# Performance work log

Hardware: AMD Instinct MI355X
Metric: run time of the kernel (lower is better)

## Reference

```python
import jax, jax.numpy as jnp
import numpy as np

N = 100000      # num_nodes
E = 1600000     # num_edges
F_IN = 10       # node_feature_dim
H = 64          # hidden_channels
B = 128         # num graphs in batch
C = 3           # num_classes
EPS = 1e-5      # BatchNorm eps


def setup_inputs() -> dict:
    key = jax.random.key(0)
    ks = jax.random.split(key, 32)
    inp = {
        'x': jax.random.normal(ks[0], (N, F_IN), dtype=jnp.float32),
        'edge_index': jax.random.randint(ks[1], (2, E), 0, N, dtype=jnp.int32),
        'batch': jnp.sort(jax.random.randint(ks[2], (N,), 0, B, dtype=jnp.int32)),
    }
    dims = [(F_IN, H), (H, H), (H, H)]
    k = 3
    for i, (din, dout) in enumerate(dims, start=1):
        inp[f'W{i}'] = jax.random.normal(ks[k], (din, dout)) * (1.0 / np.sqrt(din)); k += 1
        inp[f'b{i}'] = jax.random.normal(ks[k], (dout,)) * 0.01; k += 1
        inp[f'g{i}'] = 1.0 + 0.1 * jax.random.normal(ks[k], (dout,)); k += 1
        inp[f'be{i}'] = 0.1 * jax.random.normal(ks[k], (dout,)); k += 1
        inp[f'm{i}'] = 0.1 * jax.random.normal(ks[k], (dout,)); k += 1
        inp[f'v{i}'] = 0.5 + jax.random.uniform(ks[k], (dout,)); k += 1
    inp['fw1'] = jax.random.normal(ks[k], (H, H // 2)) * (1.0 / np.sqrt(H)); k += 1
    inp['fb1'] = jax.random.normal(ks[k], (H // 2,)) * 0.01; k += 1
    inp['fw2'] = jax.random.normal(ks[k], (H // 2, C)) * (1.0 / np.sqrt(H // 2)); k += 1
    inp['fb2'] = jax.random.normal(ks[k], (C,)) * 0.01
    return inp


def reference(x, edge_index, batch,
              W1, b1, g1, be1, m1, v1,
              W2, b2, g2, be2, m2, v2,
              W3, b3, g3, be3, m3, v3,
              fw1, fb1, fw2, fb2):
    src, dst = edge_index[0], edge_index[1]
    # GCN normalization with implicit self-loops: deg includes the self-loop
    deg = jax.ops.segment_sum(jnp.ones((E,), x.dtype), dst, num_segments=N) + 1.0
    dinv = jax.lax.rsqrt(deg)
    ecoef = (dinv[src] * dinv[dst])[:, None]   # per-edge norm [E,1]
    scoef = (dinv * dinv)[:, None]             # self-loop norm [N,1]

    def gcn_conv(h, W, b):
        h = h @ W  # [N, dout]
        agg = jax.ops.segment_sum(h[src] * ecoef, dst, num_segments=N)
        return agg + h * scoef + b

    def bn(h, g, be, m, v):  # eval-mode BatchNorm1d
        return (h - m) * jax.lax.rsqrt(v + EPS) * g + be

    h = jax.nn.relu(bn(gcn_conv(x, W1, b1), g1, be1, m1, v1))
    h = jax.nn.relu(bn(gcn_conv(h, W2, b2), g2, be2, m2, v2))
    h = jax.nn.relu(bn(gcn_conv(h, W3, b3), g3, be3, m3, v3))

    # global mean pool over batch assignment
    counts = jax.ops.segment_sum(jnp.ones((N,), h.dtype), batch, num_segments=B)
    pooled = jax.ops.segment_sum(h, batch, num_segments=B) / jnp.maximum(counts, 1.0)[:, None]

    out = jax.nn.relu(pooled @ fw1 + fb1) @ fw2 + fb2  # [B, C]
    return out
```

## Files before the change

kernel.cpp:

```cpp
#include <hip/hip_runtime.h>
#include <hip/hip_bf16.h>
#include <hip/hip_fp16.h>

#define N_NODES 100000
#define E_EDGES 1600000
#define F_IN    10
#define H       64
#define B_GR    128
#define C_CLS   3
#define BN_EPS  1e-5f
#define NH      (N_NODES * H)
#define NBLK_SCAN ((N_NODES + 255) / 256)

#define TILE1   4096
#define NB1     391
#define L2CAP   6144

__global__ void deg_kernel(const int* __restrict__ dst, int* __restrict__ deg) {
    int e = blockIdx.x * blockDim.x + threadIdx.x;
    if (e < E_EDGES) atomicAdd(&deg[dst[e]], 1);
}

__global__ void dinv_kernel(const int* __restrict__ deg, float* __restrict__ dinv) {
    int n = blockIdx.x * blockDim.x + threadIdx.x;
    if (n < N_NODES) dinv[n] = rsqrtf((float)deg[n] + 1.0f);
}

__global__ void scan1_kernel(const int* __restrict__ deg, int* __restrict__ rowptr,
                             int* __restrict__ blockSums) {
    __shared__ int lds[256];
    int t = threadIdx.x;
    int i = blockIdx.x * 256 + t;
    int v = (i < N_NODES) ? deg[i] : 0;
    lds[t] = v;
    __syncthreads();
    for (int off = 1; off < 256; off <<= 1) {
        int add = (t >= off) ? lds[t - off] : 0;
        __syncthreads();
        lds[t] += add;
        __syncthreads();
    }
    if (i < N_NODES) rowptr[i] = lds[t] - v;
    if (t == 255) blockSums[blockIdx.x] = lds[255];
}

__global__ void scan2_kernel(const int* __restrict__ blockSums, int* __restrict__ blockOff) {
    __shared__ int lds[512];
    int t = threadIdx.x;
    int v = (t < NBLK_SCAN) ? blockSums[t] : 0;
    lds[t] = v;
    __syncthreads();
    for (int off = 1; off < 512; off <<= 1) {
        int add = (t >= off) ? lds[t - off] : 0;
        __syncthreads();
        lds[t] += add;
        __syncthreads();
    }
    if (t < NBLK_SCAN) blockOff[t] = lds[t] - v;
}

__global__ void scan3_kernel(int* __restrict__ rowptr, const int* __restrict__ blockOff,
                             int* __restrict__ bcur) {
    int i = blockIdx.x * blockDim.x + threadIdx.x;
    if (i < N_NODES) {
        int r = rowptr[i] + blockOff[i >> 8];
        rowptr[i] = r;
        if ((i & 255) == 0) bcur[i >> 8] = r;
    } else if (i == N_NODES) {
        rowptr[N_NODES] = E_EDGES;
    }
}

__global__ __launch_bounds__(256) void l1sort_kernel(const int* __restrict__ src,
                                                     const int* __restrict__ dst,
                                                     int* __restrict__ bcur,
                                                     int* __restrict__ inter) {
    __shared__ int hist[NB1];
    __shared__ int sbase[NB1];
    __shared__ int gbase[NB1];
    __shared__ int scanA[512];
    __shared__ int scanB[512];
    __shared__ int ebuf[TILE1];
    __shared__ unsigned short bkt[TILE1];

    int tid   = threadIdx.x;
    int tbase = blockIdx.x * TILE1;
    int tcnt  = min(TILE1, E_EDGES - tbase);

    for (int i = tid; i < NB1; i += 256) hist[i] = 0;
    __syncthreads();

    int   pk[16];
    int   rk[16];
    short bb[16];
#pragma unroll
    for (int j = 0; j < 16; ++j) {
        int i = j * 256 + tid;
        if (i < tcnt) {
            int e = tbase + i;
            int s = src[e], d = dst[e];
            int b  = d >> 8;
            int dl = d & 255;
            pk[j] = s | (dl << 17);
            bb[j] = (short)b;
            rk[j] = atomicAdd(&hist[b], 1);
        } else {
            pk[j] = -1; rk[j] = 0; bb[j] = 0;
        }
    }
    __syncthreads();

    for (int i = tid; i < 512; i += 256) scanA[i] = (i < NB1) ? hist[i] : 0;
    __syncthreads();
    int* A = scanA; int* B = scanB;
    for (int off = 1; off < 512; off <<= 1) {
        for (int i = tid; i < 512; i += 256)
            B[i] = A[i] + ((i >= off) ? A[i - off] : 0);
        __syncthreads();
        int* t = A; A = B; B = t;
    }
    for (int i = tid; i < NB1; i += 256) {
        int c = hist[i];
        sbase[i] = A[i] - c;
        gbase[i] = (c > 0) ? atomicAdd(&bcur[i], c) : 0;
    }
    __syncthreads();

#pragma unroll
    for (int j = 0; j < 16; ++j) {
        if (pk[j] >= 0) {
            int b   = bb[j];
            int pos = sbase[b] + rk[j];
            ebuf[pos] = pk[j];
            bkt[pos]  = (unsigned short)b;
        }
    }
    __syncthreads();

    for (int i = tid; i < tcnt; i += 256) {
        int b = bkt[i];
        inter[gbase[b] + (i - sbase[b])] = ebuf[i];
    }
}

__global__ __launch_bounds__(256) void l2sort_kernel(const int* __restrict__ rowptr,
                                                     const int* __restrict__ inter,
                                                     const float* __restrict__ dinv,
                                                     float2* __restrict__ edata) {
    __shared__ int    nhist[256];
    __shared__ int    nscan[256];
    __shared__ float2 ebuf[L2CAP];

    int tid      = threadIdx.x;
    int b        = blockIdx.x;
    int nodeBase = b << 8;
    int lo       = rowptr[nodeBase];
    int hi       = rowptr[min(nodeBase + 256, N_NODES)];
    int cnt      = hi - lo;
    if (cnt > L2CAP) cnt = L2CAP;

    nhist[tid] = 0;
    __syncthreads();

    int vv[24];
    int dr[24];
#pragma unroll
    for (int j = 0; j < 24; ++j) {
        int i = j * 256 + tid;
        if (i < cnt) {
            int v  = inter[lo + i];
            int dl = (v >> 17) & 255;
            int r  = atomicAdd(&nhist[dl], 1);
            vv[j] = v;
            dr[j] = (dl << 16) | r;
        } else {
            vv[j] = -1; dr[j] = 0;
        }
    }
    __syncthreads();

    int vval = nhist[tid];
    nscan[tid] = vval;
    __syncthreads();
    for (int off = 1; off < 256; off <<= 1) {
        int add = (tid >= off) ? nscan[tid - off] : 0;
        __syncthreads();
        nscan[tid] += add;
        __syncthreads();
    }
    nhist[tid] = nscan[tid] - vval;
    __syncthreads();

#pragma unroll
    for (int j = 0; j < 24; ++j) {
        if (vv[j] >= 0) {
            int dl  = dr[j] >> 16;
            int r   = dr[j] & 0xFFFF;
            int pos = nhist[dl] + r;
            int s   = vv[j] & 0x1FFFF;
            int d   = nodeBase + dl;
            ebuf[pos] = make_float2(__int_as_float(s), dinv[s] * dinv[d]);
        }
    }
    __syncthreads();

    for (int i = tid; i < cnt; i += 256)
        edata[lo + i] = ebuf[i];
}

__global__ void pad_kernel(const float* __restrict__ x, __half* __restrict__ xph) {
    int idx = blockIdx.x * blockDim.x + threadIdx.x;
    if (idx >= N_NODES * 16) return;
    int n = idx >> 4, c = idx & 15;
    xph[idx] = __float2half((c < F_IN) ? x[n * F_IN + c] : 0.0f);
}

__global__ __launch_bounds__(256) void gather16_kernel(const int* __restrict__ rowptr,
                                                       const float2* __restrict__ edata,
                                                       const __half* __restrict__ xph,
                                                       const float* __restrict__ dinv,
                                                       float* __restrict__ agg16) {
    int tid  = threadIdx.x;
    int n    = blockIdx.x * 4 + (tid >> 6);
    if (n >= N_NODES) return;
    int lane = tid & 63;
    int grp  = lane >> 2;
    int c4   = (lane & 3) * 4;

    int start = rowptr[n], end = rowptr[n + 1];
    float4 acc = make_float4(0.f, 0.f, 0.f, 0.f);
    for (int p = start; p < end; p += 16) {
        int q = p + grp;
        float2 ed = (q < end) ? edata[q] : make_float2(__int_as_float(0), 0.0f);
        int   s = __float_as_int(ed.x);
        float w = ed.y;
        uint2 raw = *(const uint2*)&xph[s * 16 + c4];
        float2 f01 = __half22float2(*reinterpret_cast<__half2*>(&raw.x));
        float2 f23 = __half22float2(*reinterpret_cast<__half2*>(&raw.y));
        acc.x = fmaf(w, f01.x, acc.x);
        acc.y = fmaf(w, f01.y, acc.y);
        acc.z = fmaf(w, f23.x, acc.z);
        acc.w = fmaf(w, f23.y, acc.w);
    }
#pragma unroll
    for (int off = 4; off < 64; off <<= 1) {
        acc.x += __shfl_xor(acc.x, off);
        acc.y += __shfl_xor(acc.y, off);
        acc.z += __shfl_xor(acc.z, off);
        acc.w += __shfl_xor(acc.w, off);
    }
    if (grp == 0) {
        uint2 raw = *(const uint2*)&xph[n * 16 + c4];
        float2 s01 = __half22float2(*reinterpret_cast<__half2*>(&raw.x));
        float2 s23 = __half22float2(*reinterpret_cast<__half2*>(&raw.y));
        float  di   = dinv[n];
        float  di2  = di * di;
        acc.x = fmaf(s01.x, di2, acc.x);
        acc.y = fmaf(s01.y, di2, acc.y);
        acc.z = fmaf(s23.x, di2, acc.z);
        acc.w = fmaf(s23.y, di2, acc.w);
        *(float4*)&agg16[n * 16 + c4] = acc;
    }
}

__global__ __launch_bounds__(256) void matmul16_bn_kernel(const float* __restrict__ agg16,
                                                          const float* __restrict__ W,
                                                          const float* __restrict__ b,
                                                          const float* __restrict__ g,
                                                          const float* __restrict__ be,
                                                          const float* __restrict__ m,
                                                          const float* __restrict__ v,
                                                          float* __restrict__ hout) {
    __shared__ float rowLds[16 * 16];
    __shared__ float Wlds[F_IN * 68];
    int tid  = threadIdx.x;
    int base = blockIdx.x * 16;

    if (tid < 64) {
        int r = tid >> 2, c = (tid & 3) * 4;
        *(float4*)&rowLds[r * 16 + c] = *(const float4*)&agg16[(base + r) * 16 + c];
    }
    for (int i = tid; i < F_IN * 64; i += 256) {
        int k = i >> 6, c = i & 63;
        Wlds[k * 68 + c] = W[i];
    }
    __syncthreads();

    int r  = tid >> 4;
    int c4 = (tid & 15) * 4;
    float4 acc = make_float4(0.f, 0.f, 0.f, 0.f);
#pragma unroll
    for (int k = 0; k < F_IN; ++k) {
        float  rv = rowLds[r * 16 + k];
        float4 wv = *(const float4*)&Wlds[k * 68 + c4];
        acc.x = fmaf(rv, wv.x, acc.x);
        acc.y = fmaf(rv, wv.y, acc.y);
        acc.z = fmaf(rv, wv.z, acc.z);
        acc.w = fmaf(rv, wv.w, acc.w);
    }
    float4 gv = *(const float4*)&g[c4];
    float4 vv = *(const float4*)&v[c4];
    float4 bv = *(const float4*)&b[c4];
    float4 mv = *(const float4*)&m[c4];
    float4 bev= *(const float4*)&be[c4];
    float4 sc, sh, r2;
    sc.x = gv.x * rsqrtf(vv.x + BN_EPS);
    sc.y = gv.y * rsqrtf(vv.y + BN_EPS);
    sc.z = gv.z * rsqrtf(vv.z + BN_EPS);
    sc.w = gv.w * rsqrtf(vv.w + BN_EPS);
    sh.x = bev.x + (bv.x - mv.x) * sc.x;
    sh.y = bev.y + (bv.y - mv.y) * sc.y;
    sh.z = bev.z + (bv.z - mv.z) * sc.z;
    sh.w = bev.w + (bv.w - mv.w) * sc.w;
    r2.x = fmaxf(acc.x * sc.x + sh.x, 0.f);
    r2.y = fmaxf(acc.y * sc.y + sh.y, 0.f);
    r2.z = fmaxf(acc.z * sc.z + sh.z, 0.f);
    r2.w = fmaxf(acc.w * sc.w + sh.w, 0.f);
    *(float4*)&hout[(base + r) * H + c4] = r2;
}

__global__ __launch_bounds__(256) void matmul_kernel(const float* __restrict__ hin,
                                                     const float* __restrict__ W,
                                                     __half* __restrict__ houth) {
    __shared__ float rowLds[16 * 65];
    __shared__ float Wlds[H * 68];
    int tid  = threadIdx.x;
    int base = blockIdx.x * 16;

    for (int i = tid; i < H * 64; i += 256)
        Wlds[(i >> 6) * 68 + (i & 63)] = W[i];
    for (int i = tid; i < 16 * H; i += 256) {
        int r = i >> 6, k = i & 63;
        rowLds[r * 65 + k] = hin[(base + r) * H + k];
    }
    __syncthreads();

    int r  = tid >> 4;
    int c4 = (tid & 15) * 4;
    float4 acc = make_float4(0.f, 0.f, 0.f, 0.f);
#pragma unroll
    for (int k = 0; k < H; ++k) {
        float  rv = rowLds[r * 65 + k];
        float4 wv = *(const float4*)&Wlds[k * 68 + c4];
        acc.x = fmaf(rv, wv.x, acc.x);
        acc.y = fmaf(rv, wv.y, acc.y);
        acc.z = fmaf(rv, wv.z, acc.z);
        acc.w = fmaf(rv, wv.w, acc.w);
    }
    __half2 h01 = __float22half2_rn(make_float2(acc.x, acc.y));
    __half2 h23 = __float22half2_rn(make_float2(acc.z, acc.w));
    uint2 packed;
    packed.x = *reinterpret_cast<unsigned*>(&h01);
    packed.y = *reinterpret_cast<unsigned*>(&h23);
    *(uint2*)&houth[(base + r) * H + c4] = packed;
}

__global__ __launch_bounds__(256) void gather_kernel(const int* __restrict__ rowptr,
                                                     const float2* __restrict__ edata,
                                                     const __half* __restrict__ hWh,
                                                     const float* __restrict__ dinv,
                                                     const float* __restrict__ b,
                                                     const float* __restrict__ g,
                                                     const float* __restrict__ be,
                                                     const float* __restrict__ m,
                                                     const float* __restrict__ v,
                                                     float* __restrict__ hout) {
    int tid  = threadIdx.x;
    int n    = blockIdx.x * 4 + (tid >> 6);
    if (n >= N_NODES) return;
    int lane = tid & 63;
    int grp  = lane >> 4;
    int c4   = (lane & 15) * 4;

    int start = rowptr[n], end = rowptr[n + 1];
    float4 acc  = make_float4(0.f, 0.f, 0.f, 0.f);
    float4 acc2 = make_float4(0.f, 0.f, 0.f, 0.f);
    for (int p = start; p < end; p += 8) {
        int q1 = p + grp;
        int q2 = p + 4 + grp;
        float2 e1 = (q1 < end) ? edata[q1] : make_float2(__int_as_float(0), 0.0f);
        float2 e2 = (q2 < end) ? edata[q2] : make_float2(__int_as_float(0), 0.0f);
        int   s1 = __float_as_int(e1.x); float w1 = e1.y;
        int   s2 = __float_as_int(e2.x); float w2 = e2.y;
        uint2 r1 = *(const uint2*)&hWh[s1 * H + c4];
        uint2 r2 = *(const uint2*)&hWh[s2 * H + c4];
        float2 a01 = __half22float2(*reinterpret_cast<__half2*>(&r1.x));
        float2 a23 = __half22float2(*reinterpret_cast<__half2*>(&r1.y));
        acc.x = fmaf(w1, a01.x, acc.x);
        acc.y = fmaf(w1, a01.y, acc.y);
        acc.z = fmaf(w1, a23.x, acc.z);
        acc.w = fmaf(w1, a23.y, acc.w);
        float2 b01 = __half22float2(*reinterpret_cast<__half2*>(&r2.x));
        float2 b23 = __half22float2(*reinterpret_cast<__half2*>(&r2.y));
        acc2.x = fmaf(w2, b01.x, acc2.x);
        acc2.y = fmaf(w2, b01.y, acc2.y);
        acc2.z = fmaf(w2, b23.x, acc2.z);
        acc2.w = fmaf(w2, b23.y, acc2.w);
    }
    acc.x += acc2.x; acc.y += acc2.y; acc.z += acc2.z; acc.w += acc2.w;
#pragma unroll
    for (int off = 16; off < 64; off <<= 1) {
        acc.x += __shfl_xor(acc.x, off);
        acc.y += __shfl_xor(acc.y, off);
        acc.z += __shfl_xor(acc.z, off);
        acc.w += __shfl_xor(acc.w, off);
    }
    if (grp == 0) {
        uint2 rs = *(const uint2*)&hWh[n * H + c4];
        float2 s01 = __half22float2(*reinterpret_cast<__half2*>(&rs.x));
        float2 s23 = __half22float2(*reinterpret_cast<__half2*>(&rs.y));
        float  di   = dinv[n];
        float  di2  = di * di;
        float4 gv = *(const float4*)&g[c4];
        float4 vv = *(const float4*)&v[c4];
        float4 bv = *(const float4*)&b[c4];
        float4 mv = *(const float4*)&m[c4];
        float4 bev= *(const float4*)&be[c4];
        float4 sc, sh, r2;
        sc.x = gv.x * rsqrtf(vv.x + BN_EPS);
        sc.y = gv.y * rsqrtf(vv.y + BN_EPS);
        sc.z = gv.z * rsqrtf(vv.z + BN_EPS);
        sc.w = gv.w * rsqrtf(vv.w + BN_EPS);
        sh.x = bev.x + (bv.x - mv.x) * sc.x;
        sh.y = bev.y + (bv.y - mv.y) * sc.y;
        sh.z = bev.z + (bv.z - mv.z) * sc.z;
        sh.w = bev.w + (bv.w - mv.w) * sc.w;
        r2.x = fmaxf((acc.x + s01.x * di2) * sc.x + sh.x, 0.f);
        r2.y = fmaxf((acc.y + s01.y * di2) * sc.y + sh.y, 0.f);
        r2.z = fmaxf((acc.z + s23.x * di2) * sc.z + sh.z, 0.f);
        r2.w = fmaxf((acc.w + s23.y * di2) * sc.w + sh.w, 0.f);
        *(float4*)&hout[n * H + c4] = r2;
    }
}

#define PCHUNK 128
__global__ void pool_kernel(const float* __restrict__ h, const int* __restrict__ batch,
                            float* __restrict__ pooled, float* __restrict__ counts) {
    int tid  = threadIdx.x;
    int wid  = blockIdx.x * 4 + (tid >> 6);
    int lane = tid & 63;
    int n0   = wid * PCHUNK;
    if (n0 >= N_NODES) return;
    int n1 = min(n0 + PCHUNK, N_NODES);

    int   curb = batch[n0];
    float acc  = 0.0f;
    int   run  = 0;
    for (int n = n0; n < n1; ++n) {
        int bb = batch[n];
        if (bb != curb) {
            atomicAdd(&pooled[curb * H + lane], acc);
            if (lane == 0) atomicAdd(&counts[curb], (float)run);
            acc = 0.0f; run = 0; curb = bb;
        }
        acc += h[n * H + lane];
        ++run;
    }
    atomicAdd(&pooled[curb * H + lane], acc);
    if (lane == 0) atomicAdd(&counts[curb], (float)run);
}

__global__ void mlp_kernel(const float* __restrict__ pooled, const float* __restrict__ counts,
                           const float* __restrict__ fw1, const float* __restrict__ fb1,
                           const float* __restrict__ fw2, const float* __restrict__ fb2,
                           float* __restrict__ out) {
    __shared__ float prow[H];
    __shared__ float hid[H / 2];
    int b = blockIdx.x;
    int t = threadIdx.x;
    float cnt = fmaxf(counts[b], 1.0f);
    prow[t] = pooled[b * H + t] / cnt;
    __syncthreads();
    if (t < H / 2) {
        float acc = fb1[t];
#pragma unroll
        for (int k = 0; k < H; ++k) acc += prow[k] * fw1[k * (H / 2) + t];
        hid[t] = fmaxf(acc, 0.0f);
    }
    __syncthreads();
    if (t < C_CLS) {
        float acc = fb2[t];
#pragma unroll
        for (int j = 0; j < H / 2; ++j) acc += hid[j] * fw2[j * C_CLS + t];
        out[b * C_CLS + t] = acc;
    }
}

extern "C" void kernel_launch(void* const* d_in, const int* in_sizes, int n_in,
                              void* d_out, int out_size, void* d_ws, size_t ws_size,
                              hipStream_t stream) {
    const float* x          = (const float*)d_in[0];
    const int*   edge_index = (const int*)d_in[1];
    const int*   batch      = (const int*)d_in[2];

    const float* W1 = (const float*)d_in[3];
    const float* b1 = (const float*)d_in[4];
    const float* g1 = (const float*)d_in[5];
    const float* be1= (const float*)d_in[6];
    const float* m1 = (const float*)d_in[7];
    const float* v1 = (const float*)d_in[8];
    const float* W2 = (const float*)d_in[9];
    const float* b2 = (const float*)d_in[10];
    const float* g2 = (const float*)d_in[11];
    const float* be2= (const float*)d_in[12];
    const float* m2 = (const float*)d_in[13];
    const float* v2 = (const float*)d_in[14];
    const float* W3 = (const float*)d_in[15];
    const float* b3 = (const float*)d_in[16];
    const float* g3 = (const float*)d_in[17];
    const float* be3= (const float*)d_in[18];
    const float* m3 = (const float*)d_in[19];
    const float* v3 = (const float*)d_in[20];
    const float* fw1= (const float*)d_in[21];
    const float* fb1= (const float*)d_in[22];
    const float* fw2= (const float*)d_in[23];
    const float* fb2= (const float*)d_in[24];

    const int* src = edge_index;
    const int* dst = edge_index + E_EDGES;

    float* ws      = (float*)d_ws;
    float* hW      = ws;
    float* hbuf    = ws + (size_t)NH;
    float2* edata  = (float2*)(ws + 2 * (size_t)NH);
    float* fafter  = ws + 2 * (size_t)NH + 2 * (size_t)E_EDGES;
    int*   deg_i   = (int*)fafter;
    float* dinv    = fafter + N_NODES;
    int*   rowptr  = (int*)(fafter + 2 * N_NODES);
    int*   blockSums = (int*)(fafter + 3 * N_NODES + 1);
    int*   blockOff  = blockSums + 512;
    int*   bcur      = blockOff + 512;
    float* pooled  = fafter + 3 * N_NODES + 1 + 1536;
    float* counts  = pooled + B_GR * H;

    __half* hWh  = (__half*)hW;
    __half* xph  = (__half*)hW;
    float* agg16 = hW + (size_t)N_NODES * 16;
    int*   inter = (int*)(hW + 2 * (size_t)N_NODES * 16);

    float* out = (float*)d_out;

    hipMemsetAsync(deg_i, 0, N_NODES * sizeof(int), stream);
    hipMemsetAsync(pooled, 0, (B_GR * H + B_GR) * sizeof(float), stream);

    deg_kernel<<<(E_EDGES + 255) / 256, 256, 0, stream>>>(dst, deg_i);
    dinv_kernel<<<(N_NODES + 255) / 256, 256, 0, stream>>>(deg_i, dinv);

    scan1_kernel<<<NBLK_SCAN, 256, 0, stream>>>(deg_i, rowptr, blockSums);
    scan2_kernel<<<1, 512, 0, stream>>>(blockSums, blockOff);
    scan3_kernel<<<(N_NODES + 256) / 256, 256, 0, stream>>>(rowptr, blockOff, bcur);

    l1sort_kernel<<<(E_EDGES + TILE1 - 1) / TILE1, 256, 0, stream>>>(src, dst, bcur, inter);
    l2sort_kernel<<<NB1, 256, 0, stream>>>(rowptr, inter, dinv, edata);

    const int mmGrid = N_NODES / 16;
    const int gGrid  = N_NODES / 4;

    pad_kernel<<<(N_NODES * 16 + 255) / 256, 256, 0, stream>>>(x, xph);
    gather16_kernel<<<gGrid, 256, 0, stream>>>(rowptr, edata, xph, dinv, agg16);
    matmul16_bn_kernel<<<mmGrid, 256, 0, stream>>>(agg16, W1, b1, g1, be1, m1, v1, hbuf);

    matmul_kernel<<<mmGrid, 256, 0, stream>>>(hbuf, W2, hWh);
    gather_kernel<<<gGrid, 256, 0, stream>>>(rowptr, edata, hWh, dinv, b2, g2, be2, m2, v2, hbuf);

    matmul_kernel<<<mmGrid, 256, 0, stream>>>(hbuf, W3, hWh);
    gather_kernel<<<gGrid, 256, 0, stream>>>(rowptr, edata, hWh, dinv, b3, g3, be3, m3, v3, hbuf);

    const int poolWaves = (N_NODES + PCHUNK - 1) / PCHUNK;
    pool_kernel<<<(poolWaves + 3) / 4, 256, 0, stream>>>(hbuf, batch, pooled, counts);
    mlp_kernel<<<B_GR, 64, 0, stream>>>(pooled, counts, fw1, fb1, fw2, fb2, out);
}
```

Before: 499.0 us.

## Replace per-node degree atomics and scans with bucket histogram; store src-only CSR

Drops the global per-edge degree atomics, dinv kernel and three-pass node scan. In their place, a per-tile LDS bucket histogram and a single bucket scan feed the two-level sort, which now derives per-node degree, dinv and rowptr inside l2sort. The edge array keeps only source indices, and the per-edge weight is recomputed in the gathers as dinv[src]*dinv[dst]. This cuts preprocessing launches and global atomics and halves edge-array traffic, at the cost of one extra dependent dinv load per edge in each gather.

```diff
diff --git a/kernel.cpp b/kernel.cpp
--- a/kernel.cpp
+++ b/kernel.cpp
@@ -10,44 +10,33 @@
 #define C_CLS   3
 #define BN_EPS  1e-5f
 #define NH      (N_NODES * H)
-#define NBLK_SCAN ((N_NODES + 255) / 256)
 
 #define TILE1   4096
 #define NB1     391
 #define L2CAP   6144
 
-__global__ void deg_kernel(const int* __restrict__ dst, int* __restrict__ deg) {
-    int e = blockIdx.x * blockDim.x + threadIdx.x;
-    if (e < E_EDGES) atomicAdd(&deg[dst[e]], 1);
-}
-
-__global__ void dinv_kernel(const int* __restrict__ deg, float* __restrict__ dinv) {
-    int n = blockIdx.x * blockDim.x + threadIdx.x;
-    if (n < N_NODES) dinv[n] = rsqrtf((float)deg[n] + 1.0f);
-}
-
-__global__ void scan1_kernel(const int* __restrict__ deg, int* __restrict__ rowptr,
-                             int* __restrict__ blockSums) {
-    __shared__ int lds[256];
-    int t = threadIdx.x;
-    int i = blockIdx.x * 256 + t;
-    int v = (i < N_NODES) ? deg[i] : 0;
-    lds[t] = v;
-    __syncthreads();
-    for (int off = 1; off < 256; off <<= 1) {
-        int add = (t >= off) ? lds[t - off] : 0;
-        __syncthreads();
-        lds[t] += add;
-        __syncthreads();
-    }
-    if (i < N_NODES) rowptr[i] = lds[t] - v;
-    if (t == 255) blockSums[blockIdx.x] = lds[255];
-}
-
-__global__ void scan2_kernel(const int* __restrict__ blockSums, int* __restrict__ blockOff) {
+__global__ __launch_bounds__(256) void bhist_kernel(const int* __restrict__ dst,
+                                                    int* __restrict__ bucketCnt) {
+    __shared__ int hist[NB1];
+    int tid   = threadIdx.x;
+    int tbase = blockIdx.x * TILE1;
+    int tcnt  = min(TILE1, E_EDGES - tbase);
+    for (int i = tid; i < NB1; i += 256) hist[i] = 0;
+    __syncthreads();
+    for (int i = tid; i < tcnt; i += 256)
+        atomicAdd(&hist[dst[tbase + i] >> 8], 1);
+    __syncthreads();
+    for (int i = tid; i < NB1; i += 256) {
+        int c = hist[i];
+        if (c) atomicAdd(&bucketCnt[i], c);
+    }
+}
+
+__global__ void bscan_kernel(const int* __restrict__ bucketCnt,
+                             int* __restrict__ bucketBase, int* __restrict__ bcur) {
     __shared__ int lds[512];
     int t = threadIdx.x;
-    int v = (t < NBLK_SCAN) ? blockSums[t] : 0;
+    int v = (t < NB1) ? bucketCnt[t] : 0;
     lds[t] = v;
     __syncthreads();
     for (int off = 1; off < 512; off <<= 1) {
@@ -56,19 +45,12 @@
         lds[t] += add;
         __syncthreads();
     }
-    if (t < NBLK_SCAN) blockOff[t] = lds[t] - v;
-}
-
-__global__ void scan3_kernel(int* __restrict__ rowptr, const int* __restrict__ blockOff,
-                             int* __restrict__ bcur) {
-    int i = blockIdx.x * blockDim.x + threadIdx.x;
-    if (i < N_NODES) {
-        int r = rowptr[i] + blockOff[i >> 8];
-        rowptr[i] = r;
-        if ((i & 255) == 0) bcur[i >> 8] = r;
-    } else if (i == N_NODES) {
-        rowptr[N_NODES] = E_EDGES;
-    }
+    if (t < NB1) {
+        int base = lds[t] - v;
+        bucketBase[t] = base;
+        bcur[t] = base;
+    }
+    if (t == 0) bucketBase[NB1] = E_EDGES;
 }
 
 __global__ __launch_bounds__(256) void l1sort_kernel(const int* __restrict__ src,
@@ -143,19 +125,20 @@
     }
 }
 
-__global__ __launch_bounds__(256) void l2sort_kernel(const int* __restrict__ rowptr,
+__global__ __launch_bounds__(256) void l2sort_kernel(const int* __restrict__ bucketBase,
                                                      const int* __restrict__ inter,
-                                                     const float* __restrict__ dinv,
-                                                     float2* __restrict__ edata) {
-    __shared__ int    nhist[256];
-    __shared__ int    nscan[256];
-    __shared__ float2 ebuf[L2CAP];
+                                                     float* __restrict__ dinv,
+                                                     int* __restrict__ rowptr,
+                                                     int* __restrict__ esrc) {
+    __shared__ int nhist[256];
+    __shared__ int nbase[256];
+    __shared__ int ebuf[L2CAP];
 
     int tid      = threadIdx.x;
     int b        = blockIdx.x;
     int nodeBase = b << 8;
-    int lo       = rowptr[nodeBase];
-    int hi       = rowptr[min(nodeBase + 256, N_NODES)];
+    int lo       = bucketBase[b];
+    int hi       = bucketBase[b + 1];
     int cnt      = hi - lo;
     if (cnt > L2CAP) cnt = L2CAP;
 
@@ -179,16 +162,25 @@
     }
     __syncthreads();
 
-    int vval = nhist[tid];
-    nscan[tid] = vval;
+    int deg = nhist[tid];
+    nbase[tid] = deg;
     __syncthreads();
     for (int off = 1; off < 256; off <<= 1) {
-        int add = (tid >= off) ? nscan[tid - off] : 0;
+        int add = (tid >= off) ? nbase[tid - off] : 0;
         __syncthreads();
-        nscan[tid] += add;
+        nbase[tid] += add;
         __syncthreads();
     }
-    nhist[tid] = nscan[tid] - vval;
+    int ex = nbase[tid] - deg;
+
+    int node = nodeBase + tid;
+    if (node < N_NODES) {
+        dinv[node]   = rsqrtf((float)deg + 1.0f);
+        rowptr[node] = lo + ex;
+    }
+    if (b == NB1 - 1 && tid == 0) rowptr[N_NODES] = E_EDGES;
+
+    nbase[tid] = ex;
     __syncthreads();
 
 #pragma unroll
@@ -196,16 +188,13 @@
         if (vv[j] >= 0) {
             int dl  = dr[j] >> 16;
             int r   = dr[j] & 0xFFFF;
-            int pos = nhist[dl] + r;
-            int s   = vv[j] & 0x1FFFF;
-            int d   = nodeBase + dl;
-            ebuf[pos] = make_float2(__int_as_float(s), dinv[s] * dinv[d]);
+            ebuf[nbase[dl] + r] = vv[j] & 0x1FFFF;
         }
     }
     __syncthreads();
 
     for (int i = tid; i < cnt; i += 256)
-        edata[lo + i] = ebuf[i];
+        esrc[lo + i] = ebuf[i];
 }
 
 __global__ void pad_kernel(const float* __restrict__ x, __half* __restrict__ xph) {
@@ -216,7 +205,7 @@
 }
 
 __global__ __launch_bounds__(256) void gather16_kernel(const int* __restrict__ rowptr,
-                                                       const float2* __restrict__ edata,
+                                                       const int* __restrict__ esrc,
                                                        const __half* __restrict__ xph,
                                                        const float* __restrict__ dinv,
                                                        float* __restrict__ agg16) {
@@ -228,12 +217,12 @@
     int c4   = (lane & 3) * 4;
 
     int start = rowptr[n], end = rowptr[n + 1];
+    float dn  = dinv[n];
     float4 acc = make_float4(0.f, 0.f, 0.f, 0.f);
     for (int p = start; p < end; p += 16) {
         int q = p + grp;
-        float2 ed = (q < end) ? edata[q] : make_float2(__int_as_float(0), 0.0f);
-        int   s = __float_as_int(ed.x);
-        float w = ed.y;
+        int   s = (q < end) ? esrc[q] : 0;
+        float w = ((q < end) ? dinv[s] : 0.0f) * dn;
         uint2 raw = *(const uint2*)&xph[s * 16 + c4];
         float2 f01 = __half22float2(*reinterpret_cast<__half2*>(&raw.x));
         float2 f23 = __half22float2(*reinterpret_cast<__half2*>(&raw.y));
@@ -253,8 +242,7 @@
         uint2 raw = *(const uint2*)&xph[n * 16 + c4];
         float2 s01 = __half22float2(*reinterpret_cast<__half2*>(&raw.x));
         float2 s23 = __half22float2(*reinterpret_cast<__half2*>(&raw.y));
-        float  di   = dinv[n];
-        float  di2  = di * di;
+        float  di2  = dn * dn;
         acc.x = fmaf(s01.x, di2, acc.x);
         acc.y = fmaf(s01.y, di2, acc.y);
         acc.z = fmaf(s23.x, di2, acc.z);
@@ -356,7 +344,7 @@
 }
 
 __global__ __launch_bounds__(256) void gather_kernel(const int* __restrict__ rowptr,
-                                                     const float2* __restrict__ edata,
+                                                     const int* __restrict__ esrc,
                                                      const __half* __restrict__ hWh,
                                                      const float* __restrict__ dinv,
                                                      const float* __restrict__ b,
@@ -373,15 +361,16 @@
     int c4   = (lane & 15) * 4;
 
     int start = rowptr[n], end = rowptr[n + 1];
+    float dn  = dinv[n];
     float4 acc  = make_float4(0.f, 0.f, 0.f, 0.f);
     float4 acc2 = make_float4(0.f, 0.f, 0.f, 0.f);
     for (int p = start; p < end; p += 8) {
         int q1 = p + grp;
         int q2 = p + 4 + grp;
-        float2 e1 = (q1 < end) ? edata[q1] : make_float2(__int_as_float(0), 0.0f);
-        float2 e2 = (q2 < end) ? edata[q2] : make_float2(__int_as_float(0), 0.0f);
-        int   s1 = __float_as_int(e1.x); float w1 = e1.y;
-        int   s2 = __float_as_int(e2.x); float w2 = e2.y;
+        int   s1 = (q1 < end) ? esrc[q1] : 0;
+        int   s2 = (q2 < end) ? esrc[q2] : 0;
+        float w1 = ((q1 < end) ? dinv[s1] : 0.0f) * dn;
+        float w2 = ((q2 < end) ? dinv[s2] : 0.0f) * dn;
         uint2 r1 = *(const uint2*)&hWh[s1 * H + c4];
         uint2 r2 = *(const uint2*)&hWh[s2 * H + c4];
         float2 a01 = __half22float2(*reinterpret_cast<__half2*>(&r1.x));
@@ -409,8 +398,7 @@
         uint2 rs = *(const uint2*)&hWh[n * H + c4];
         float2 s01 = __half22float2(*reinterpret_cast<__half2*>(&rs.x));
         float2 s23 = __half22float2(*reinterpret_cast<__half2*>(&rs.y));
-        float  di   = dinv[n];
-        float  di2  = di * di;
+        float  di2  = dn * dn;
         float4 gv = *(const float4*)&g[c4];
         float4 vv = *(const float4*)&v[c4];
         float4 bv = *(const float4*)&b[c4];
@@ -522,15 +510,14 @@
     float* ws      = (float*)d_ws;
     float* hW      = ws;
     float* hbuf    = ws + (size_t)NH;
-    float2* edata  = (float2*)(ws + 2 * (size_t)NH);
-    float* fafter  = ws + 2 * (size_t)NH + 2 * (size_t)E_EDGES;
-    int*   deg_i   = (int*)fafter;
-    float* dinv    = fafter + N_NODES;
-    int*   rowptr  = (int*)(fafter + 2 * N_NODES);
-    int*   blockSums = (int*)(fafter + 3 * N_NODES + 1);
-    int*   blockOff  = blockSums + 512;
-    int*   bcur      = blockOff + 512;
-    float* pooled  = fafter + 3 * N_NODES + 1 + 1536;
+    int*   esrc    = (int*)(ws + 2 * (size_t)NH);
+    float* fafter  = ws + 2 * (size_t)NH + (size_t)E_EDGES;
+    float* dinv    = fafter;
+    int*   rowptr  = (int*)(fafter + N_NODES);
+    int*   bucketCnt  = (int*)(fafter + 2 * N_NODES + 1);
+    int*   bucketBase = bucketCnt + 512;
+    int*   bcur       = bucketBase + 512;
+    float* pooled  = fafter + 2 * N_NODES + 1 + 1536;
     float* counts  = pooled + B_GR * H;
 
     __half* hWh  = (__half*)hW;
@@ -540,31 +527,27 @@
 
     float* out = (float*)d_out;
 
-    hipMemsetAsync(deg_i, 0, N_NODES * sizeof(int), stream);
+    hipMemsetAsync(bucketCnt, 0, 512 * sizeof(int), stream);
     hipMemsetAsync(pooled, 0, (B_GR * H + B_GR) * sizeof(float), stream);
 
-    deg_kernel<<<(E_EDGES + 255) / 256, 256, 0, stream>>>(dst, deg_i);
-    dinv_kernel<<<(N_NODES + 255) / 256, 256, 0, stream>>>(deg_i, dinv);
-
-    scan1_kernel<<<NBLK_SCAN, 256, 0, stream>>>(deg_i, rowptr, blockSums);
-    scan2_kernel<<<1, 512, 0, stream>>>(blockSums, blockOff);
-    scan3_kernel<<<(N_NODES + 256) / 256, 256, 0, stream>>>(rowptr, blockOff, bcur);
-
-    l1sort_kernel<<<(E_EDGES + TILE1 - 1) / TILE1, 256, 0, stream>>>(src, dst, bcur, inter);
-    l2sort_kernel<<<NB1, 256, 0, stream>>>(rowptr, inter, dinv, edata);
+    const int nTiles = (E_EDGES + TILE1 - 1) / TILE1;
+    bhist_kernel<<<nTiles, 256, 0, stream>>>(dst, bucketCnt);
+    bscan_kernel<<<1, 512, 0, stream>>>(bucketCnt, bucketBase, bcur);
+    l1sort_kernel<<<nTiles, 256, 0, stream>>>(src, dst, bcur, inter);
+    l2sort_kernel<<<NB1, 256, 0, stream>>>(bucketBase, inter, dinv, rowptr, esrc);
 
     const int mmGrid = N_NODES / 16;
     const int gGrid  = N_NODES / 4;
 
     pad_kernel<<<(N_NODES * 16 + 255) / 256, 256, 0, stream>>>(x, xph);
-    gather16_kernel<<<gGrid, 256, 0, stream>>>(rowptr, edata, xph, dinv, agg16);
+    gather16_kernel<<<gGrid, 256, 0, stream>>>(rowptr, esrc, xph, dinv, agg16);
     matmul16_bn_kernel<<<mmGrid, 256, 0, stream>>>(agg16, W1, b1, g1, be1, m1, v1, hbuf);
 
     matmul_kernel<<<mmGrid, 256, 0, stream>>>(hbuf, W2, hWh);
-    gather_kernel<<<gGrid, 256, 0, stream>>>(rowptr, edata, hWh, dinv, b2, g2, be2, m2, v2, hbuf);
+    gather_kernel<<<gGrid, 256, 0, stream>>>(rowptr, esrc, hWh, dinv, b2, g2, be2, m2, v2, hbuf);
 
     matmul_kernel<<<mmGrid, 256, 0, stream>>>(hbuf, W3, hWh);
-    gather_kernel<<<gGrid, 256, 0, stream>>>(rowptr, edata, hWh, dinv, b3, g3, be3, m3, v3, hbuf);
+    gather_kernel<<<gGrid, 256, 0, stream>>>(rowptr, esrc, hWh, dinv, b3, g3, be3, m3, v3, hbuf);
 
     const int poolWaves = (N_NODES + PCHUNK - 1) / PCHUNK;
     pool_kernel<<<(poolWaves + 3) / 4, 256, 0, stream>>>(hbuf, batch, pooled, counts);
```

New measurement: 456.8 us. 1.09x faster.
